# Kernel optimization log

Hardware: AMD Instinct MI355X
Metric: run time of the kernel (lower is better)

## Reference

```python
import jax, jax.numpy as jnp
import numpy as np

CHUNK = 64
L2_EPS = 1e-6
RMS_EPS = 1e-5


def _silu(x):
    return x * jax.nn.sigmoid(x)


def _causal_shared_conv(x, w):
    # x: [B,T,C]; w: [K] single kernel shared across all channels (depthwise).
    K = w.shape[0]
    T = x.shape[1]
    xp = jnp.pad(x, ((0, 0), (K - 1, 0), (0, 0)))
    out = w[0] * xp[:, 0:T, :]
    for j in range(1, K):  # K=4, tiny fixed loop
        out = out + w[j] * xp[:, j:j + T, :]
    return out


def _l2norm(x):
    return x * jax.lax.rsqrt(jnp.sum(x * x, axis=-1, keepdims=True) + L2_EPS)


def _delta_rule_chunk(q, k, v, beta, chunk=CHUNK):
    # q,k: [B,H,T,dk]; v: [B,H,T,dv]; beta: [B,H,T]
    B, H, T, dk = q.shape
    dv = v.shape[-1]
    q = q * (dk ** -0.5)
    nC = T // chunk
    q = q.reshape(B, H, nC, chunk, dk)
    k = k.reshape(B, H, nC, chunk, dk)
    v = v.reshape(B, H, nC, chunk, dv)
    beta = beta.reshape(B, H, nC, chunk)
    k_beta = k * beta[..., None]
    v_beta = v * beta[..., None]
    # UT transform: invert the unit-lower-triangular (I + stril(K_beta K^T))
    A = jnp.einsum('bhncd,bhnmd->bhncm', k_beta, k)  # [B,H,nC,C,C]
    stril = jnp.tril(jnp.ones((chunk, chunk), bool), -1)
    M = jnp.where(stril, A, 0.0) + jnp.eye(chunk, dtype=q.dtype)
    u = jax.scipy.linalg.solve_triangular(M, v_beta, lower=True)  # T @ (beta*v)
    w = jax.scipy.linalg.solve_triangular(M, k_beta, lower=True)  # T @ (beta*k)
    tril_incl = jnp.tril(jnp.ones((chunk, chunk), bool))

    def step(S, inp):
        q_i, k_i, u_i, w_i = inp  # [B,H,C,d*]
        u_i = u_i - jnp.einsum('bhcd,bhde->bhce', w_i, S)
        attn = jnp.where(tril_incl, jnp.einsum('bhcd,bhmd->bhcm', q_i, k_i), 0.0)
        o_i = jnp.einsum('bhcd,bhde->bhce', q_i, S) + jnp.einsum('bhcm,bhme->bhce', attn, u_i)
        S = S + jnp.einsum('bhcd,bhce->bhde', k_i, u_i)
        return S, o_i

    xs = tuple(jnp.moveaxis(t, 2, 0) for t in (q, k, u, w))
    S0 = jnp.zeros((B, H, dk, dv), q.dtype)
    _, o = jax.lax.scan(step, S0, xs)  # o: [nC,B,H,C,dv]
    return jnp.moveaxis(o, 0, 2).reshape(B, H, T, dv)


def setup_inputs() -> dict:
    key = jax.random.key(0)
    ks = jax.random.split(key, 10)
    B, T, D, H = 2, 4096, 2048, 16
    sc = 0.02
    return {
        'x': jax.random.normal(ks[0], (B, T, D), jnp.float32),
        'Wq': jax.random.normal(ks[1], (D, D), jnp.float32) * sc,
        'Wk': jax.random.normal(ks[2], (D, D), jnp.float32) * sc,
        'Wv': jax.random.normal(ks[3], (D, D), jnp.float32) * sc,
        'Wb': jax.random.normal(ks[4], (D, H), jnp.float32) * sc,
        'Wo': jax.random.normal(ks[5], (D, D), jnp.float32) * sc,
        'conv_q': jax.random.normal(ks[6], (4,), jnp.float32) * 0.5,
        'conv_k': jax.random.normal(ks[7], (4,), jnp.float32) * 0.5,
        'conv_v': jax.random.normal(ks[8], (4,), jnp.float32) * 0.5,
        'onorm_w': jnp.ones((D // H,), jnp.float32),
    }


def reference(x, Wq, Wk, Wv, Wb, Wo, conv_q, conv_k, conv_v, onorm_w):
    B, T, D = x.shape
    H = Wb.shape[1]
    dk = Wq.shape[1] // H
    dv = Wv.shape[1] // H
    # projections + shared-kernel causal short conv (silu activation)
    q = _silu(_causal_shared_conv(x @ Wq, conv_q))
    k = _silu(_causal_shared_conv(x @ Wk, conv_k))
    v = _silu(_causal_shared_conv(x @ Wv, conv_v))
    beta = jax.nn.sigmoid(x @ Wb)  # [B,T,H]
    # split heads -> [B,H,T,d]
    qh = _l2norm(q.reshape(B, T, H, dk)).transpose(0, 2, 1, 3)
    kh = _l2norm(k.reshape(B, T, H, dk)).transpose(0, 2, 1, 3)
    vh = v.reshape(B, T, H, dv).transpose(0, 2, 1, 3)
    o = _delta_rule_chunk(qh, kh, vh, beta.transpose(0, 2, 1))  # [B,H,T,dv]
    o = o.transpose(0, 2, 1, 3)  # [B,T,H,dv]
    # per-head RMSNorm over head_v_dim
    o = o * jax.lax.rsqrt(jnp.mean(o * o, axis=-1, keepdims=True) + RMS_EPS) * onorm_w
    return o.reshape(B, T, H * dv) @ Wo
```

## Files before the change

### kernel.cpp

```cpp
#include <hip/hip_runtime.h>
#include <math.h>

#define B_ 2
#define T_ 4096
#define D_ 2048
#define H_ 16
#define DK 128
#define DV 128
#define CH 64
#define M_ (B_ * T_)
#define NCH (T_ / CH)

typedef __attribute__((ext_vector_type(8))) short bfrag;
typedef __attribute__((ext_vector_type(4))) float ffrag;
typedef __attribute__((ext_vector_type(8))) unsigned short u16x8;
typedef unsigned short us;

#define MFMA __builtin_amdgcn_mfma_f32_16x16x32_bf16

__device__ inline us f2bf(float f) {
  union { float f; unsigned u; } v; v.f = f;
  unsigned r = v.u + 0x7fffu + ((v.u >> 16) & 1u);
  return (us)(r >> 16);
}
__device__ inline float bf2f(us u) {
  union { unsigned u; float f; } v; v.u = ((unsigned)u) << 16;
  return v.f;
}

__device__ inline void gl_lds16(const us* g, us* l) {
  __builtin_amdgcn_global_load_lds(
      (const __attribute__((address_space(1))) void*)g,
      (__attribute__((address_space(3))) void*)l, 16, 0, 0);
}

__global__ __launch_bounds__(256) void to_bf16(const float* __restrict__ in,
                                               us* __restrict__ out) {
  const size_t i = ((size_t)blockIdx.x * 256 + threadIdx.x) * 8;
  const float4 a = *reinterpret_cast<const float4*>(in + i);
  const float4 b = *reinterpret_cast<const float4*>(in + i + 4);
  ushort4 o0, o1;
  o0.x = f2bf(a.x); o0.y = f2bf(a.y); o0.z = f2bf(a.z); o0.w = f2bf(a.w);
  o1.x = f2bf(b.x); o1.y = f2bf(b.y); o1.z = f2bf(b.z); o1.w = f2bf(b.w);
  *reinterpret_cast<ushort4*>(out + i) = o0;
  *reinterpret_cast<ushort4*>(out + i + 4) = o1;
}

__global__ __launch_bounds__(256) void wtrans(const float* __restrict__ W,
                                              us* __restrict__ Wt) {
  __shared__ float tile[64][68];
  const int k0 = blockIdx.y * 64, n0 = blockIdx.x * 64;
  const int lr = threadIdx.x >> 4, lc = (threadIdx.x & 15) * 4;
#pragma unroll
  for (int p = 0; p < 4; ++p) {
    const int r = lr + p * 16;
    *reinterpret_cast<float4*>(&tile[r][lc]) =
        *reinterpret_cast<const float4*>(&W[(size_t)(k0 + r) * D_ + n0 + lc]);
  }
  __syncthreads();
#pragma unroll
  for (int p = 0; p < 4; ++p) {
    const int r = lr + p * 16;
    ushort4 o;
    o.x = f2bf(tile[lc + 0][r]); o.y = f2bf(tile[lc + 1][r]);
    o.z = f2bf(tile[lc + 2][r]); o.w = f2bf(tile[lc + 3][r]);
    *reinterpret_cast<ushort4*>(&Wt[(size_t)(n0 + r) * D_ + k0 + lc]) = o;
  }
}

template <bool OUTF32>
__global__ __launch_bounds__(512, 2) void gemm256(const us* __restrict__ A,
                                                  const us* __restrict__ Bt,
                                                  void* __restrict__ Cp,
                                                  int M, int N, int K) {
  __shared__ __align__(16) us lA[3][256 * 32];
  __shared__ __align__(16) us lB[3][256 * 32];
  const int t = threadIdx.x, l = t & 63, w = t >> 6;
  const int wm = w >> 2, wn = w & 3;
  const int fr = l & 15, hi = l >> 4;
  const int colx = 8 * (hi ^ ((fr >> 2) & 3));

  const int nx = gridDim.x;
  const int nwg = nx * gridDim.y;
  const int lin = blockIdx.y * nx + blockIdx.x;
  const int swz = (lin & 7) * (nwg >> 3) + (lin >> 3);
  const int m0 = (swz / nx) * 256, n0 = (swz % nx) * 256;

  const int srow = t >> 2;
  const int csrc = ((t & 3) * 8) ^ (((t >> 4) & 3) * 8);
  const us* Asrc0 = A + (size_t)(m0 + srow) * K + csrc;
  const us* Asrc1 = A + (size_t)(m0 + 128 + srow) * K + csrc;
  const us* Bsrc0 = Bt + (size_t)(n0 + srow) * K + csrc;
  const us* Bsrc1 = Bt + (size_t)(n0 + 128 + srow) * K + csrc;

  ffrag acc[8][4];
#pragma unroll
  for (int mi = 0; mi < 8; ++mi)
#pragma unroll
    for (int ni = 0; ni < 4; ++ni)
#pragma unroll
      for (int e = 0; e < 4; ++e) acc[mi][ni][e] = 0.f;

#define SA_(bufp, g)                                              \
  do {                                                            \
    gl_lds16(Asrc0 + (size_t)(g) * 32, (bufp) + t * 8);           \
    gl_lds16(Asrc1 + (size_t)(g) * 32, (bufp) + 4096 + t * 8);    \
  } while (0)
#define SB_(bufp, g)                                              \
  do {                                                            \
    gl_lds16(Bsrc0 + (size_t)(g) * 32, (bufp) + t * 8);           \
    gl_lds16(Bsrc1 + (size_t)(g) * 32, (bufp) + 4096 + t * 8);    \
  } while (0)

  const int NT = K >> 5;
  us* const baseA = &lA[0][0];
  us* const baseB = &lB[0][0];

  SA_(baseA, 0); SB_(baseB, 0);
  SA_(baseA + 8192, 1); SB_(baseB + 8192, 1);
  asm volatile("s_waitcnt vmcnt(4)" ::: "memory");
  __builtin_amdgcn_s_barrier();
  __builtin_amdgcn_sched_barrier(0);

  int cur = 0, nxt = 2;
  const int rbA = wm * 128 + fr;
  const int rbB = wn * 64 + fr;

#pragma unroll 1
  for (int g = 0; g < NT; ++g) {
    us* const curA = baseA + cur * 8192;
    us* const curB = baseB + cur * 8192;
    us* const nxtA = baseA + nxt * 8192;
    us* const nxtB = baseB + nxt * 8192;

    bfrag bf4[4], af4[4];
#pragma unroll
    for (int ni = 0; ni < 4; ++ni)
      bf4[ni] = *reinterpret_cast<const bfrag*>(curB + (rbB + ni * 16) * 32 + colx);
#pragma unroll
    for (int mi = 0; mi < 4; ++mi)
      af4[mi] = *reinterpret_cast<const bfrag*>(curA + (rbA + mi * 16) * 32 + colx);
    if (g + 2 < NT) SA_(nxtA, g + 2);
    __builtin_amdgcn_s_barrier();
    asm volatile("s_waitcnt lgkmcnt(0)" ::: "memory");
    __builtin_amdgcn_sched_barrier(0);
    __builtin_amdgcn_s_setprio(1);
#pragma unroll
    for (int mi = 0; mi < 4; ++mi)
#pragma unroll
      for (int ni = 0; ni < 4; ++ni)
        acc[mi][ni] = MFMA(af4[mi], bf4[ni], acc[mi][ni], 0, 0, 0);
    __builtin_amdgcn_s_setprio(0);
    __builtin_amdgcn_s_barrier();

#pragma unroll
    for (int mi = 0; mi < 4; ++mi)
      af4[mi] = *reinterpret_cast<const bfrag*>(curA + (rbA + (mi + 4) * 16) * 32 + colx);
    if (g + 2 < NT) SB_(nxtB, g + 2);
    __builtin_amdgcn_s_barrier();
    asm volatile("s_waitcnt lgkmcnt(0)" ::: "memory");
    __builtin_amdgcn_sched_barrier(0);
    __builtin_amdgcn_s_setprio(1);
#pragma unroll
    for (int mi = 0; mi < 4; ++mi)
#pragma unroll
      for (int ni = 0; ni < 4; ++ni)
        acc[mi + 4][ni] = MFMA(af4[mi], bf4[ni], acc[mi + 4][ni], 0, 0, 0);
    __builtin_amdgcn_s_setprio(0);
    if (g + 2 < NT)
      asm volatile("s_waitcnt vmcnt(4)" ::: "memory");
    else
      asm volatile("s_waitcnt vmcnt(0)" ::: "memory");
    __builtin_amdgcn_s_barrier();
    __builtin_amdgcn_sched_barrier(0);

    cur = (cur == 2) ? 0 : cur + 1;
    nxt = (nxt == 2) ? 0 : nxt + 1;
  }
#undef SA_
#undef SB_

  const int crow = m0 + wm * 128 + 4 * hi;
  const int ccol = n0 + wn * 64 + fr;
#pragma unroll
  for (int mi = 0; mi < 8; ++mi)
#pragma unroll
    for (int ni = 0; ni < 4; ++ni)
#pragma unroll
      for (int j = 0; j < 4; ++j) {
        const size_t idx = (size_t)(crow + mi * 16 + j) * N + ccol + ni * 16;
        if constexpr (OUTF32) ((float*)Cp)[idx] = acc[mi][ni][j];
        else ((us*)Cp)[idx] = f2bf(acc[mi][ni][j]);
      }
}

__device__ inline void conv_body(const us* __restrict__ in, const float* cw,
                                 int bt, int d0, int mode, float v[8]) {
  const int tb = bt & (T_ - 1);
  const us* row = in + (size_t)bt * D_ + d0;
#pragma unroll
  for (int j = 0; j < 8; ++j) v[j] = 0.f;
#pragma unroll
  for (int j = 0; j < 4; ++j) {
    if (tb >= j) {
      const us* rp = row - (size_t)(j * D_);
      const ushort4 a = *reinterpret_cast<const ushort4*>(rp);
      const ushort4 b = *reinterpret_cast<const ushort4*>(rp + 4);
      const float wj = cw[3 - j];
      v[0] = fmaf(wj, bf2f(a.x), v[0]); v[1] = fmaf(wj, bf2f(a.y), v[1]);
      v[2] = fmaf(wj, bf2f(a.z), v[2]); v[3] = fmaf(wj, bf2f(a.w), v[3]);
      v[4] = fmaf(wj, bf2f(b.x), v[4]); v[5] = fmaf(wj, bf2f(b.y), v[5]);
      v[6] = fmaf(wj, bf2f(b.z), v[6]); v[7] = fmaf(wj, bf2f(b.w), v[7]);
    }
  }
#pragma unroll
  for (int j = 0; j < 8; ++j) v[j] = v[j] / (1.f + expf(-v[j]));
  if (mode) {
    float ss = 0.f;
#pragma unroll
    for (int j = 0; j < 8; ++j) ss = fmaf(v[j], v[j], ss);
    ss += __shfl_xor(ss, 1);
    ss += __shfl_xor(ss, 2);
    ss += __shfl_xor(ss, 4);
    ss += __shfl_xor(ss, 8);
    float sc = rsqrtf(ss + 1e-6f);
    if (mode == 2) sc *= 0.08838834764831845f;
#pragma unroll
    for (int j = 0; j < 8; ++j) v[j] *= sc;
  }
}

__global__ __launch_bounds__(256) void conv_silu_plain(const us* __restrict__ in,
                                                       const float* __restrict__ cw,
                                                       us* __restrict__ out) {
  const int bt = blockIdx.x, d0 = threadIdx.x * 8;
  float v[8];
  conv_body(in, cw, bt, d0, 0, v);
  ushort4 o0, o1;
  o0.x = f2bf(v[0]); o0.y = f2bf(v[1]); o0.z = f2bf(v[2]); o0.w = f2bf(v[3]);
  o1.x = f2bf(v[4]); o1.y = f2bf(v[5]); o1.z = f2bf(v[6]); o1.w = f2bf(v[7]);
  us* op = out + (size_t)bt * D_ + d0;
  *reinterpret_cast<ushort4*>(op) = o0;
  *reinterpret_cast<ushort4*>(op + 4) = o1;
}

__global__ __launch_bounds__(256) void conv_silu_chunk(const us* __restrict__ in,
                                                       const float* __restrict__ cw,
                                                       us* __restrict__ out,
                                                       int mode) {
  const int bt = blockIdx.x, d0 = threadIdx.x * 8;
  float v[8];
  conv_body(in, cw, bt, d0, mode, v);
  const int b = bt >> 12, tt = bt & (T_ - 1);
  const int cid = tt >> 6, r = tt & 63;
  const int h = d0 >> 7, g = (d0 & 127) >> 3;
  us* dst = out + ((size_t)((b * H_ + h) * NCH + cid)) * (CH * DK) +
            r * 128 + ((g ^ (r & 15)) * 8);
  ushort4 o0, o1;
  o0.x = f2bf(v[0]); o0.y = f2bf(v[1]); o0.z = f2bf(v[2]); o0.w = f2bf(v[3]);
  o1.x = f2bf(v[4]); o1.y = f2bf(v[5]); o1.z = f2bf(v[6]); o1.w = f2bf(v[7]);
  *reinterpret_cast<ushort4*>(dst) = o0;
  *reinterpret_cast<ushort4*>(dst + 4) = o1;
}

__global__ __launch_bounds__(256) void beta_sigmoid(const float* __restrict__ x,
                                                    const float* __restrict__ Wb,
                                                    float* __restrict__ betaT) {
  const int t = threadIdx.x;
  const int m = blockIdx.x * 4 + (t >> 6);
  const int l = t & 63;
  const int c = l & 15;
  const int s = l >> 4;
  const float* xr = x + (size_t)m * D_;
  const int kb = s * (D_ / 4);
  float acc = 0.f;
  for (int k = 0; k < D_ / 4; ++k)
    acc = fmaf(xr[kb + k], Wb[(size_t)(kb + k) * H_ + c], acc);
  acc += __shfl_xor(acc, 16);
  acc += __shfl_xor(acc, 32);
  if (l < 16) {
    const int b = m >> 12, tt = m & (T_ - 1);
    betaT[((size_t)(b * H_ + c)) * T_ + tt] = 1.f / (1.f + expf(-acc));
  }
}

__device__ inline void prod_step(float* Tf, const float* Am, float* xbuf,
                                 int r, int c, int I, int J,
                                 int nk, int K0, int K1, int K2) {
  float X = 0.f;
  const int Ks[3] = {K0, K1, K2};
  for (int kk = 0; kk < nk; ++kk) {
    const int K = Ks[kk];
    const float* amrow = Am + (16 * I + r) * 72 + 16 * K;
    const float* tcol = Tf + (16 * K) * 68 + 16 * J + c;
#pragma unroll
    for (int m = 0; m < 16; ++m) X = fmaf(amrow[m], tcol[m * 68], X);
  }
  __syncthreads();
  xbuf[r * 17 + c] = X;
  __syncthreads();
  float s = 0.f;
  const float* trow = Tf + (16 * I + r) * 68 + 16 * I;
#pragma unroll
  for (int m = 0; m < 16; ++m) s = fmaf(trow[m], xbuf[m * 17 + c], s);
  Tf[(16 * I + r) * 68 + 16 * J + c] = -s;
  __syncthreads();
}

__global__ __launch_bounds__(256, 2) void delta_prep(const us* __restrict__ qch,
                                                     const us* __restrict__ kch,
                                                     const float* __restrict__ betaT,
                                                     us* __restrict__ v_uv,
                                                     us* __restrict__ Wout,
                                                     us* __restrict__ kTout,
                                                     us* __restrict__ Aout) {
  __shared__ __align__(16) unsigned char lds[72000];
  us*    ks    = (us*)(lds);
  us*    Tb    = (us*)(lds);
  float* Am    = (float*)(lds + 16384);
  us*    vTb   = (us*)(lds + 16384);
  float* Tf    = (float*)(lds + 34816);
  us*    atst  = (us*)(lds + 34816);
  us*    Wst   = (us*)(lds + 34816);
  us*    kTb   = (us*)(lds + 52224);
  us*    UVst  = (us*)(lds + 52224);
  float* betac = (float*)(lds + 70656);
  float* xbuf  = (float*)(lds + 70912);

  const int t = threadIdx.x, w = t >> 6, l = t & 63;
  const int rr = l & 15, hi = l >> 4;
  const int bx = blockIdx.x;
  const int bh = bx >> 6, cid = bx & 63;
  const int b = bh >> 4, h = bh & 15;
  const size_t rowbase = ((size_t)b * T_ + (size_t)cid * CH) * D_ + (size_t)h * DK;
  const size_t cbase = (size_t)bx * (CH * DK);
  const size_t abase = (size_t)bx * (CH * CH);

  {
    const us* kg = kch + cbase;
#pragma unroll
    for (int p = 0; p < 4; ++p)
      gl_lds16(kg + p * 2048 + t * 8, ks + p * 2048 + t * 8);
    const float4 z = make_float4(0.f, 0.f, 0.f, 0.f);
    *reinterpret_cast<float4*>(atst + t * 16) = z;
    *reinterpret_cast<float4*>(atst + t * 16 + 8) = z;
    if (t < 64) betac[t] = betaT[(size_t)bh * T_ + cid * CH + t];
  }
  __syncthreads();

  {
    bfrag qf[4], kf[4];
#pragma unroll
    for (int k4 = 0; k4 < 4; ++k4) {
      const int go = ((4 * k4 + hi) ^ rr) * 8;
      qf[k4] = *reinterpret_cast<const bfrag*>(qch + cbase + (16 * w + rr) * 128 + go);
      kf[k4] = *reinterpret_cast<const bfrag*>(ks + (16 * w + rr) * 128 + go);
    }
    for (int jt = 0; jt <= w; ++jt) {
      ffrag accA = {0.f, 0.f, 0.f, 0.f}, accQ = {0.f, 0.f, 0.f, 0.f};
#pragma unroll
      for (int k4 = 0; k4 < 4; ++k4) {
        const bfrag bfr = *reinterpret_cast<const bfrag*>(
            ks + (16 * jt + rr) * 128 + (((4 * k4 + hi) ^ rr) * 8));
        accA = MFMA(kf[k4], bfr, accA, 0, 0, 0);
        accQ = MFMA(qf[k4], bfr, accQ, 0, 0, 0);
      }
#pragma unroll
      for (int j4 = 0; j4 < 4; ++j4) {
        const int i = 16 * w + 4 * hi + j4, j = 16 * jt + rr;
        Am[i * 72 + j] = (j < i) ? betac[i] * accA[j4] : 0.f;
        if (j <= i)
          atst[i * 64 + (((j >> 3) ^ (i & 7)) * 8) + (j & 7)] = f2bf(accQ[j4]);
      }
    }
    const int r = t & 63, part = t >> 6;
#pragma unroll
    for (int gi = 0; gi < 4; ++gi) {
      const int g = 4 * part + gi;
      const u16x8 kv = *reinterpret_cast<const u16x8*>(ks + r * 128 + ((g ^ (r & 15)) * 8));
#pragma unroll
      for (int j = 0; j < 8; ++j) kTb[(g * 8 + j) * 72 + r] = kv[j];
    }
  }
  __syncthreads();

  {
#pragma unroll
    for (int p = 0; p < 2; ++p) {
      const int unit = t + p * 256;
      *reinterpret_cast<u16x8*>(Aout + abase + unit * 8) =
          *reinterpret_cast<const u16x8*>(atst + unit * 8);
    }
#pragma unroll
    for (int p = 0; p < 4; ++p) {
      const int unit = t + p * 256;
      const int d = unit >> 3, sg = unit & 7;
      *reinterpret_cast<u16x8*>(kTout + cbase + unit * 8) =
          *reinterpret_cast<const u16x8*>(kTb + d * 72 + ((sg ^ (d & 7)) * 8));
    }
  }
  __syncthreads();
  for (int i = t; i < 64 * 68; i += 256) Tf[i] = 0.f;
  __syncthreads();

  if (t < 64) {
    const int blk = t >> 4, j = t & 15, bd = blk * 16;
    Tf[(bd + j) * 68 + bd + j] = 1.f;
    for (int i = j + 1; i < 16; ++i) {
      float s = 0.f;
      for (int m = j; m < i; ++m)
        s = fmaf(Am[(bd + i) * 72 + bd + m], Tf[(bd + m) * 68 + bd + j], s);
      Tf[(bd + i) * 68 + bd + j] = -s;
    }
  }
  __syncthreads();

  {
    const int r = t >> 4, c = t & 15;
    prod_step(Tf, Am, xbuf, r, c, 1, 0, 1, 0, 0, 0);
    prod_step(Tf, Am, xbuf, r, c, 2, 0, 2, 0, 1, 0);
    prod_step(Tf, Am, xbuf, r, c, 3, 0, 3, 0, 1, 2);
    prod_step(Tf, Am, xbuf, r, c, 2, 1, 1, 1, 0, 0);
    prod_step(Tf, Am, xbuf, r, c, 3, 1, 2, 1, 2, 0);
    prod_step(Tf, Am, xbuf, r, c, 3, 2, 1, 2, 0, 0);
  }

  {
    const int vr = t >> 2, vp = t & 3;
    u16x8 vv[4];
#pragma unroll
    for (int g = 0; g < 4; ++g)
      vv[g] = *reinterpret_cast<const u16x8*>(v_uv + rowbase + (size_t)vr * D_ +
                                              vp * 32 + g * 8);
    const int ti = t >> 2, tg = t & 3;
    u16x8 w0, w1;
#pragma unroll
    for (int jj = 0; jj < 8; ++jj) {
      const int j0 = tg * 16 + jj, j1 = j0 + 8;
      w0[jj] = f2bf(Tf[ti * 68 + j0] * betac[j0]);
      w1[jj] = f2bf(Tf[ti * 68 + j1] * betac[j1]);
    }
    *reinterpret_cast<u16x8*>(Tb + ti * 72 + tg * 16) = w0;
    *reinterpret_cast<u16x8*>(Tb + ti * 72 + tg * 16 + 8) = w1;
#pragma unroll
    for (int g = 0; g < 4; ++g)
#pragma unroll
      for (int j = 0; j < 8; ++j)
        vTb[(vp * 32 + g * 8 + j) * 72 + vr] = vv[g][j];
  }
  __syncthreads();

  {
    bfrag ta[2];
#pragma unroll
    for (int k2 = 0; k2 < 2; ++k2)
      ta[k2] = *reinterpret_cast<const bfrag*>(Tb + (16 * w + rr) * 72 + 32 * k2 + 8 * hi);
#pragma unroll
    for (int dt = 0; dt < 8; ++dt) {
      ffrag acc = {0.f, 0.f, 0.f, 0.f};
#pragma unroll
      for (int k2 = 0; k2 < 2; ++k2) {
        const bfrag bfr = *reinterpret_cast<const bfrag*>(
            kTb + (16 * dt + rr) * 72 + 32 * k2 + 8 * hi);
        acc = MFMA(ta[k2], bfr, acc, 0, 0, 0);
      }
#pragma unroll
      for (int j4 = 0; j4 < 4; ++j4) {
        const int i = 16 * w + 4 * hi + j4, d = 16 * dt + rr;
        Wst[i * 128 + (((d >> 3) ^ (i & 15)) * 8) + (d & 7)] = f2bf(-acc[j4]);
      }
    }
  }
  __syncthreads();

  {
    bfrag ta[2];
#pragma unroll
    for (int k2 = 0; k2 < 2; ++k2)
      ta[k2] = *reinterpret_cast<const bfrag*>(Tb + (16 * w + rr) * 72 + 32 * k2 + 8 * hi);
#pragma unroll
    for (int et = 0; et < 8; ++et) {
      ffrag acc = {0.f, 0.f, 0.f, 0.f};
#pragma unroll
      for (int k2 = 0; k2 < 2; ++k2) {
        const bfrag bfr = *reinterpret_cast<const bfrag*>(
            vTb + (16 * et + rr) * 72 + 32 * k2 + 8 * hi);
        acc = MFMA(ta[k2], bfr, acc, 0, 0, 0);
      }
#pragma unroll
      for (int j4 = 0; j4 < 4; ++j4)
        UVst[(16 * w + 4 * hi + j4) * 128 + 16 * et + rr] = f2bf(acc[j4]);
    }
#pragma unroll
    for (int p = 0; p < 4; ++p) {
      const int unit = t + p * 256;
      *reinterpret_cast<u16x8*>(Wout + cbase + unit * 8) =
          *reinterpret_cast<const u16x8*>(Wst + unit * 8);
    }
  }
  __syncthreads();

#pragma unroll
  for (int p = 0; p < 4; ++p) {
    const int unit = t + p * 256;
    const int r = unit >> 4, g = unit & 15;
    *reinterpret_cast<u16x8*>(v_uv + rowbase + (size_t)r * D_ + g * 8) =
        *reinterpret_cast<const u16x8*>(UVst + r * 128 + g * 8);
  }
}

__global__ __launch_bounds__(256, 1) void delta_seq(const us* __restrict__ qch,
                                                    const us* __restrict__ Wch,
                                                    const us* __restrict__ kTch,
                                                    const us* __restrict__ atch,
                                                    us* __restrict__ uv_o) {
  __shared__ __align__(16) us qs[2][CH * DK];
  __shared__ __align__(16) us Ws[2][CH * DK];
  __shared__ __align__(16) us kTs[2][DK * CH];
  __shared__ __align__(16) us ats[2][CH * CH];
  __shared__ __align__(16) us uvs[2][CH * 16];
  __shared__ __align__(16) us Sb[2][16 * 136];
  __shared__ __align__(16) us ub[CH * 18];

  const int t = threadIdx.x, l = t & 63, w = t >> 6;
  const int bx = blockIdx.x;
  const int vs = bx >> 5, bh = bx & 31;
  const int b = bh >> 4, h = bh & 15;
  const int rr = l & 15, hi = l >> 4;

  ffrag sacc[2];
#pragma unroll
  for (int t2 = 0; t2 < 2; ++t2)
#pragma unroll
    for (int j = 0; j < 4; ++j) sacc[t2][j] = 0.f;

  for (int i = t; i < 16 * 136; i += 256) Sb[0][i] = 0;

  const size_t cbQ = (size_t)(bh * NCH) * (CH * DK);
  const size_t cbA = (size_t)(bh * NCH) * (CH * CH);
  const size_t rowbase0 = ((size_t)b * T_) * D_ + (size_t)h * DK + vs * 16;

#define STAGE(buf, cid)                                                        \
  do {                                                                         \
    const us* qg = qch + cbQ + (size_t)(cid) * (CH * DK);                      \
    const us* Wg = Wch + cbQ + (size_t)(cid) * (CH * DK);                      \
    const us* kg = kTch + cbQ + (size_t)(cid) * (CH * DK);                     \
    const us* ag = atch + cbA + (size_t)(cid) * (CH * CH);                     \
    _Pragma("unroll")                                                          \
    for (int p = 0; p < 4; ++p) {                                              \
      gl_lds16(qg + p * 2048 + t * 8, &qs[buf][p * 2048 + t * 8]);             \
      gl_lds16(Wg + p * 2048 + t * 8, &Ws[buf][p * 2048 + t * 8]);             \
      gl_lds16(kg + p * 2048 + t * 8, &kTs[buf][p * 2048 + t * 8]);            \
    }                                                                          \
    _Pragma("unroll")                                                          \
    for (int p = 0; p < 2; ++p)                                                \
      gl_lds16(ag + p * 2048 + t * 8, &ats[buf][p * 2048 + t * 8]);            \
    if (t < 128)                                                               \
      gl_lds16(uv_o + rowbase0 + (size_t)((cid) * CH + (t >> 1)) * D_ + (t & 1) * 8, \
               &uvs[buf][t * 8]);                                              \
  } while (0)

  STAGE(0, 0);
  asm volatile("s_waitcnt vmcnt(0) lgkmcnt(0)" ::: "memory");
  __builtin_amdgcn_s_barrier();
  __builtin_amdgcn_sched_barrier(0);

  for (int cid = 0; cid < NCH; ++cid) {
    const int cur = cid & 1;
    if (cid + 1 < NCH) STAGE(cur ^ 1, cid + 1);

    bfrag sbf[4];
#pragma unroll
    for (int ks = 0; ks < 4; ++ks)
      sbf[ks] = *reinterpret_cast<const bfrag*>(&Sb[cur][rr * 136 + ks * 32 + hi * 8]);

    {
      ffrag uacc;
#pragma unroll
      for (int j = 0; j < 4; ++j)
        uacc[j] = bf2f(uvs[cur][(16 * w + 4 * hi + j) * 16 + rr]);
#pragma unroll
      for (int ks = 0; ks < 4; ++ks) {
        const bfrag af = *reinterpret_cast<const bfrag*>(
            &Ws[cur][(16 * w + rr) * 128 + (((4 * ks + hi) ^ rr) * 8)]);
        uacc = MFMA(af, sbf[ks], uacc, 0, 0, 0);
      }
#pragma unroll
      for (int j = 0; j < 4; ++j)
        ub[(16 * w + 4 * hi + j) * 18 + rr] = f2bf(uacc[j]);
    }
    asm volatile("s_waitcnt lgkmcnt(0)" ::: "memory");
    __builtin_amdgcn_s_barrier();
    __builtin_amdgcn_sched_barrier(0);

    {
      ffrag oacc;
#pragma unroll
      for (int j = 0; j < 4; ++j) oacc[j] = 0.f;
#pragma unroll
      for (int ks = 0; ks < 4; ++ks) {
        const bfrag af = *reinterpret_cast<const bfrag*>(
            &qs[cur][(16 * w + rr) * 128 + (((4 * ks + hi) ^ rr) * 8)]);
        oacc = MFMA(af, sbf[ks], oacc, 0, 0, 0);
      }
      const int nks = (w < 2) ? 1 : 2;
      for (int ks = 0; ks < nks; ++ks) {
        bfrag ubf;
#pragma unroll
        for (int j = 0; j < 8; ++j)
          ubf[j] = (short)ub[(32 * ks + 8 * hi + j) * 18 + rr];
        const bfrag af = *reinterpret_cast<const bfrag*>(
            &ats[cur][(16 * w + rr) * 64 + (((4 * ks + hi) ^ (rr & 7)) * 8)]);
        oacc = MFMA(af, ubf, oacc, 0, 0, 0);
      }
      us* og = uv_o + rowbase0 + (size_t)(cid * CH) * D_;
#pragma unroll
      for (int j = 0; j < 4; ++j)
        og[(size_t)(16 * w + 4 * hi + j) * D_ + rr] = f2bf(oacc[j]);
    }

    {
      bfrag ubf[2];
#pragma unroll
      for (int ks = 0; ks < 2; ++ks)
#pragma unroll
        for (int j = 0; j < 8; ++j)
          ubf[ks][j] = (short)ub[(32 * ks + 8 * hi + j) * 18 + rr];
#pragma unroll
      for (int t2 = 0; t2 < 2; ++t2) {
        const int tile = 2 * w + t2;
#pragma unroll
        for (int ks = 0; ks < 2; ++ks) {
          const bfrag af = *reinterpret_cast<const bfrag*>(
              &kTs[cur][(16 * tile + rr) * 64 + (((4 * ks + hi) ^ (rr & 7)) * 8)]);
          sacc[t2] = MFMA(af, ubf[ks], sacc[t2], 0, 0, 0);
        }
        ushort4 sw;
        sw.x = f2bf(sacc[t2][0]); sw.y = f2bf(sacc[t2][1]);
        sw.z = f2bf(sacc[t2][2]); sw.w = f2bf(sacc[t2][3]);
        *reinterpret_cast<ushort4*>(&Sb[cur ^ 1][rr * 136 + 16 * tile + 4 * hi]) = sw;
      }
    }
    asm volatile("s_waitcnt vmcnt(0) lgkmcnt(0)" ::: "memory");
    __builtin_amdgcn_s_barrier();
    __builtin_amdgcn_sched_barrier(0);
  }
#undef STAGE
}

__global__ __launch_bounds__(256) void rms_onorm_bf16(const us* __restrict__ in,
                                                      const float* __restrict__ w,
                                                      us* __restrict__ out) {
  const int bt = blockIdx.x;
  const int d0 = threadIdx.x * 8;
  const us* p = in + (size_t)bt * D_ + d0;
  const ushort4 a = *reinterpret_cast<const ushort4*>(p);
  const ushort4 b = *reinterpret_cast<const ushort4*>(p + 4);
  float v[8] = {bf2f(a.x), bf2f(a.y), bf2f(a.z), bf2f(a.w),
                bf2f(b.x), bf2f(b.y), bf2f(b.z), bf2f(b.w)};
  float ss = 0.f;
#pragma unroll
  for (int j = 0; j < 8; ++j) ss = fmaf(v[j], v[j], ss);
  ss += __shfl_xor(ss, 1);
  ss += __shfl_xor(ss, 2);
  ss += __shfl_xor(ss, 4);
  ss += __shfl_xor(ss, 8);
  const float sc = rsqrtf(ss * (1.0f / 128.0f) + 1e-5f);
  const int hd = d0 & 127;
  ushort4 o0, o1;
  o0.x = f2bf(v[0] * sc * w[hd + 0]); o0.y = f2bf(v[1] * sc * w[hd + 1]);
  o0.z = f2bf(v[2] * sc * w[hd + 2]); o0.w = f2bf(v[3] * sc * w[hd + 3]);
  o1.x = f2bf(v[4] * sc * w[hd + 4]); o1.y = f2bf(v[5] * sc * w[hd + 5]);
  o1.z = f2bf(v[6] * sc * w[hd + 6]); o1.w = f2bf(v[7] * sc * w[hd + 7]);
  us* op = out + (size_t)bt * D_ + d0;
  *reinterpret_cast<ushort4*>(op) = o0;
  *reinterpret_cast<ushort4*>(op + 4) = o1;
}

extern "C" void kernel_launch(void* const* d_in, const int* in_sizes, int n_in,
                              void* d_out, int out_size, void* d_ws, size_t ws_size,
                              hipStream_t stream) {
  const float* x  = (const float*)d_in[0];
  const float* Wq = (const float*)d_in[1];
  const float* Wk = (const float*)d_in[2];
  const float* Wv = (const float*)d_in[3];
  const float* Wb = (const float*)d_in[4];
  const float* Wo = (const float*)d_in[5];
  const float* cq = (const float*)d_in[6];
  const float* ck = (const float*)d_in[7];
  const float* cv = (const float*)d_in[8];
  const float* ow = (const float*)d_in[9];
  float* out = (float*)d_out;

  const size_t NE = (size_t)M_ * D_;
  us* ws   = (us*)d_ws;
  us* gout = ws;
  us* qch  = ws + NE;
  us* kch  = ws + 2 * NE;
  us* Wch  = ws + 3 * NE;
  us* kTch = ws + 4 * NE;
  us* wt   = ws + 5 * NE;
  us* attb = gout;
  float* betaT = (float*)(gout + 12 * 1024 * 1024);
  us* xb = (us*)d_out;
  us* vb = xb + NE;

  dim3 gg(D_ / 256, M_ / 256);
  dim3 wg(D_ / 64, D_ / 64);

  to_bf16<<<NE / 2048, 256, 0, stream>>>(x, xb);

  wtrans<<<wg, 256, 0, stream>>>(Wv, wt);
  gemm256<false><<<gg, 512, 0, stream>>>(xb, wt, gout, M_, D_, D_);
  conv_silu_plain<<<M_, 256, 0, stream>>>(gout, cv, vb);

  wtrans<<<wg, 256, 0, stream>>>(Wq, wt);
  gemm256<false><<<gg, 512, 0, stream>>>(xb, wt, gout, M_, D_, D_);
  conv_silu_chunk<<<M_, 256, 0, stream>>>(gout, cq, qch, 2);

  wtrans<<<wg, 256, 0, stream>>>(Wk, wt);
  gemm256<false><<<gg, 512, 0, stream>>>(xb, wt, gout, M_, D_, D_);
  conv_silu_chunk<<<M_, 256, 0, stream>>>(gout, ck, kch, 1);

  beta_sigmoid<<<M_ / 4, 256, 0, stream>>>(x, Wb, betaT);

  delta_prep<<<32 * NCH, 256, 0, stream>>>(qch, kch, betaT, vb, Wch, kTch, attb);
  delta_seq<<<256, 256, 0, stream>>>(qch, Wch, kTch, attb, vb);

  rms_onorm_bf16<<<M_, 256, 0, stream>>>(vb, ow, kTch);

  wtrans<<<wg, 256, 0, stream>>>(Wo, wt);
  gemm256<true><<<gg, 512, 0, stream>>>(kTch, wt, out, M_, D_, D_);
}
```

Measured before the change: 677.7 us.

## Restructure GEMM pipeline to double-buffered 64-wide K tiles with fewer barriers

Replaces the triple-buffered 32-wide K ring in the bf16 GEMM with two buffers, each holding a 64-wide K tile split into two 32-wide halves. Each half's A and B loads are prefetched while the other half is being multiplied. This drops the barriers inside each MFMA phase, keeping one wait-and-barrier per half. It also removes the grouped workgroup-to-tile swizzle, which may hurt L2 reuse, and changes the LDS bank-conflict XOR pattern. LDS use rises from 96KB to 128KB per block.

```diff
diff --git a/kernel.cpp b/kernel.cpp
--- a/kernel.cpp
+++ b/kernel.cpp
@@ -73,25 +73,19 @@
                                                   const us* __restrict__ Bt,
                                                   void* __restrict__ Cp,
                                                   int M, int N, int K) {
-  __shared__ __align__(16) us lA[3][256 * 32];
-  __shared__ __align__(16) us lB[3][256 * 32];
+  __shared__ __align__(16) us lds[2][2][2][256 * 32];
   const int t = threadIdx.x, l = t & 63, w = t >> 6;
   const int wm = w >> 2, wn = w & 3;
   const int fr = l & 15, hi = l >> 4;
-  const int colx = 8 * (hi ^ ((fr >> 2) & 3));
-
-  const int nx = gridDim.x;
-  const int nwg = nx * gridDim.y;
-  const int lin = blockIdx.y * nx + blockIdx.x;
-  const int swz = (lin & 7) * (nwg >> 3) + (lin >> 3);
-  const int m0 = (swz / nx) * 256, n0 = (swz % nx) * 256;
+  const int sx = 8 * (hi ^ ((fr >> 1) & 3));
+
+  const int m0 = blockIdx.y * 256;
+  const int n0 = blockIdx.x * 256;
 
   const int srow = t >> 2;
-  const int csrc = ((t & 3) * 8) ^ (((t >> 4) & 3) * 8);
-  const us* Asrc0 = A + (size_t)(m0 + srow) * K + csrc;
-  const us* Asrc1 = A + (size_t)(m0 + 128 + srow) * K + csrc;
-  const us* Bsrc0 = Bt + (size_t)(n0 + srow) * K + csrc;
-  const us* Bsrc1 = Bt + (size_t)(n0 + 128 + srow) * K + csrc;
+  const int scol = 8 * ((t & 3) ^ ((t >> 3) & 3));
+  const us* Ab = A + (size_t)(m0 + srow) * K + scol;
+  const us* Bb = Bt + (size_t)(n0 + srow) * K + scol;
 
   ffrag acc[8][4];
 #pragma unroll
@@ -101,86 +95,106 @@
 #pragma unroll
       for (int e = 0; e < 4; ++e) acc[mi][ni][e] = 0.f;
 
-#define SA_(bufp, g)                                              \
-  do {                                                            \
-    gl_lds16(Asrc0 + (size_t)(g) * 32, (bufp) + t * 8);           \
-    gl_lds16(Asrc1 + (size_t)(g) * 32, (bufp) + 4096 + t * 8);    \
+#define STG_A(bf, kk, kt)                                                      \
+  do {                                                                         \
+    gl_lds16(Ab + (size_t)(kt) * 64 + (kk) * 32, &lds[bf][0][kk][t * 8]);      \
+    gl_lds16(Ab + (size_t)128 * K + (size_t)(kt) * 64 + (kk) * 32,             \
+             &lds[bf][0][kk][4096 + t * 8]);                                   \
   } while (0)
-#define SB_(bufp, g)                                              \
-  do {                                                            \
-    gl_lds16(Bsrc0 + (size_t)(g) * 32, (bufp) + t * 8);           \
-    gl_lds16(Bsrc1 + (size_t)(g) * 32, (bufp) + 4096 + t * 8);    \
+#define STG_B(bf, kk, kt)                                                      \
+  do {                                                                         \
+    gl_lds16(Bb + (size_t)(kt) * 64 + (kk) * 32, &lds[bf][1][kk][t * 8]);      \
+    gl_lds16(Bb + (size_t)128 * K + (size_t)(kt) * 64 + (kk) * 32,             \
+             &lds[bf][1][kk][4096 + t * 8]);                                   \
   } while (0)
 
-  const int NT = K >> 5;
-  us* const baseA = &lA[0][0];
-  us* const baseB = &lB[0][0];
-
-  SA_(baseA, 0); SB_(baseB, 0);
-  SA_(baseA + 8192, 1); SB_(baseB + 8192, 1);
+  const int NT = K >> 6;
+  STG_A(0, 0, 0); STG_B(0, 0, 0); STG_A(0, 1, 0); STG_B(0, 1, 0);
   asm volatile("s_waitcnt vmcnt(4)" ::: "memory");
   __builtin_amdgcn_s_barrier();
   __builtin_amdgcn_sched_barrier(0);
 
-  int cur = 0, nxt = 2;
-  const int rbA = wm * 128 + fr;
-  const int rbB = wn * 64 + fr;
+  const int arow = wm * 128 + fr;
+  const int brow = wn * 64 + fr;
 
 #pragma unroll 1
-  for (int g = 0; g < NT; ++g) {
-    us* const curA = baseA + cur * 8192;
-    us* const curB = baseB + cur * 8192;
-    us* const nxtA = baseA + nxt * 8192;
-    us* const nxtB = baseB + nxt * 8192;
-
-    bfrag bf4[4], af4[4];
-#pragma unroll
-    for (int ni = 0; ni < 4; ++ni)
-      bf4[ni] = *reinterpret_cast<const bfrag*>(curB + (rbB + ni * 16) * 32 + colx);
-#pragma unroll
-    for (int mi = 0; mi < 4; ++mi)
-      af4[mi] = *reinterpret_cast<const bfrag*>(curA + (rbA + mi * 16) * 32 + colx);
-    if (g + 2 < NT) SA_(nxtA, g + 2);
-    __builtin_amdgcn_s_barrier();
-    asm volatile("s_waitcnt lgkmcnt(0)" ::: "memory");
-    __builtin_amdgcn_sched_barrier(0);
-    __builtin_amdgcn_s_setprio(1);
-#pragma unroll
-    for (int mi = 0; mi < 4; ++mi)
+  for (int kt = 0; kt < NT; ++kt) {
+    const int cur = kt & 1, oth = cur ^ 1;
+    const bool pf = (kt + 1 < NT);
+    bfrag af4[4], bf4[4];
+
+    {
+      const us* pa = &lds[cur][0][0][0];
+      const us* pb = &lds[cur][1][0][0];
 #pragma unroll
       for (int ni = 0; ni < 4; ++ni)
-        acc[mi][ni] = MFMA(af4[mi], bf4[ni], acc[mi][ni], 0, 0, 0);
-    __builtin_amdgcn_s_setprio(0);
-    __builtin_amdgcn_s_barrier();
-
-#pragma unroll
-    for (int mi = 0; mi < 4; ++mi)
-      af4[mi] = *reinterpret_cast<const bfrag*>(curA + (rbA + (mi + 4) * 16) * 32 + colx);
-    if (g + 2 < NT) SB_(nxtB, g + 2);
-    __builtin_amdgcn_s_barrier();
-    asm volatile("s_waitcnt lgkmcnt(0)" ::: "memory");
-    __builtin_amdgcn_sched_barrier(0);
-    __builtin_amdgcn_s_setprio(1);
-#pragma unroll
-    for (int mi = 0; mi < 4; ++mi)
-#pragma unroll
-      for (int ni = 0; ni < 4; ++ni)
-        acc[mi + 4][ni] = MFMA(af4[mi], bf4[ni], acc[mi + 4][ni], 0, 0, 0);
-    __builtin_amdgcn_s_setprio(0);
-    if (g + 2 < NT)
-      asm volatile("s_waitcnt vmcnt(4)" ::: "memory");
-    else
-      asm volatile("s_waitcnt vmcnt(0)" ::: "memory");
+        bf4[ni] = *reinterpret_cast<const bfrag*>(pb + (brow + ni * 16) * 32 + sx);
+#pragma unroll
+      for (int mi = 0; mi < 4; ++mi)
+        af4[mi] = *reinterpret_cast<const bfrag*>(pa + (arow + mi * 16) * 32 + sx);
+      if (pf) STG_A(oth, 0, kt + 1);
+      __builtin_amdgcn_s_setprio(1);
+#pragma unroll
+      for (int mi = 0; mi < 4; ++mi)
+#pragma unroll
+        for (int ni = 0; ni < 4; ++ni)
+          acc[mi][ni] = MFMA(af4[mi], bf4[ni], acc[mi][ni], 0, 0, 0);
+      __builtin_amdgcn_s_setprio(0);
+#pragma unroll
+      for (int mi = 0; mi < 4; ++mi)
+        af4[mi] = *reinterpret_cast<const bfrag*>(pa + (arow + 64 + mi * 16) * 32 + sx);
+      if (pf) STG_B(oth, 0, kt + 1);
+      __builtin_amdgcn_s_setprio(1);
+#pragma unroll
+      for (int mi = 0; mi < 4; ++mi)
+#pragma unroll
+        for (int ni = 0; ni < 4; ++ni)
+          acc[mi + 4][ni] = MFMA(af4[mi], bf4[ni], acc[mi + 4][ni], 0, 0, 0);
+      __builtin_amdgcn_s_setprio(0);
+    }
+    if (pf) asm volatile("s_waitcnt vmcnt(4)" ::: "memory");
+    else    asm volatile("s_waitcnt vmcnt(0)" ::: "memory");
     __builtin_amdgcn_s_barrier();
     __builtin_amdgcn_sched_barrier(0);
 
-    cur = (cur == 2) ? 0 : cur + 1;
-    nxt = (nxt == 2) ? 0 : nxt + 1;
-  }
-#undef SA_
-#undef SB_
-
-  const int crow = m0 + wm * 128 + 4 * hi;
+    {
+      const us* pa = &lds[cur][0][1][0];
+      const us* pb = &lds[cur][1][1][0];
+#pragma unroll
+      for (int ni = 0; ni < 4; ++ni)
+        bf4[ni] = *reinterpret_cast<const bfrag*>(pb + (brow + ni * 16) * 32 + sx);
+#pragma unroll
+      for (int mi = 0; mi < 4; ++mi)
+        af4[mi] = *reinterpret_cast<const bfrag*>(pa + (arow + mi * 16) * 32 + sx);
+      if (pf) STG_A(oth, 1, kt + 1);
+      __builtin_amdgcn_s_setprio(1);
+#pragma unroll
+      for (int mi = 0; mi < 4; ++mi)
+#pragma unroll
+        for (int ni = 0; ni < 4; ++ni)
+          acc[mi][ni] = MFMA(af4[mi], bf4[ni], acc[mi][ni], 0, 0, 0);
+      __builtin_amdgcn_s_setprio(0);
+#pragma unroll
+      for (int mi = 0; mi < 4; ++mi)
+        af4[mi] = *reinterpret_cast<const bfrag*>(pa + (arow + 64 + mi * 16) * 32 + sx);
+      if (pf) STG_B(oth, 1, kt + 1);
+      __builtin_amdgcn_s_setprio(1);
+#pragma unroll
+      for (int mi = 0; mi < 4; ++mi)
+#pragma unroll
+        for (int ni = 0; ni < 4; ++ni)
+          acc[mi + 4][ni] = MFMA(af4[mi], bf4[ni], acc[mi + 4][ni], 0, 0, 0);
+      __builtin_amdgcn_s_setprio(0);
+    }
+    if (pf) asm volatile("s_waitcnt vmcnt(4)" ::: "memory");
+    else    asm volatile("s_waitcnt vmcnt(0)" ::: "memory");
+    __builtin_amdgcn_s_barrier();
+    __builtin_amdgcn_sched_barrier(0);
+  }
+#undef STG_A
+#undef STG_B
+
+  const int crow = m0 + wm * 128 + hi * 4;
   const int ccol = n0 + wn * 64 + fr;
 #pragma unroll
   for (int mi = 0; mi < 8; ++mi)
```

Result: faster. 650.9 us (-4.0%).
